# Kernel optimization log

Hardware: AMD Instinct MI355X
Metric: run time of the kernel (lower is better)

The kernel has to match this reference:

```python
import jax, jax.numpy as jnp
import numpy as np

T, N, F_IN, H1, H2, F_OUT = 48, 4096, 64, 64, 32, 64

def setup_inputs() -> dict:
    key = jax.random.key(0)
    ks = jax.random.split(key, 14)
    sc = 0.05
    x = jax.random.normal(ks[0], (T, N, F_IN), jnp.float32)
    adj = jax.random.uniform(ks[1], (N, N), jnp.float32) / N  # roughly row-normalized dense adjacency
    fc_w = jax.random.normal(ks[2], (F_IN, H1), jnp.float32) * sc
    fc_b = jnp.zeros((H1,), jnp.float32)
    Wz = jax.random.normal(ks[3], (H1, F_OUT), jnp.float32) * sc
    Wr = jax.random.normal(ks[4], (H1, F_OUT), jnp.float32) * sc
    Wh = jax.random.normal(ks[5], (H1, F_OUT), jnp.float32) * sc
    Lz = jax.random.normal(ks[6], (2 * F_OUT, F_OUT), jnp.float32) * sc
    Lr = jax.random.normal(ks[7], (2 * F_OUT, F_OUT), jnp.float32) * sc
    Lh = jax.random.normal(ks[8], (2 * F_OUT, F_OUT), jnp.float32) * sc
    bz = jnp.zeros((F_OUT,), jnp.float32)
    br = jnp.zeros((F_OUT,), jnp.float32)
    bh = jnp.zeros((F_OUT,), jnp.float32)
    return {"x": x, "adj": adj, "fc_w": fc_w, "fc_b": fc_b,
            "Wz": Wz, "Wr": Wr, "Wh": Wh,
            "Lz": Lz, "Lr": Lr, "Lh": Lh,
            "bz": bz, "br": br, "bh": bh}

def reference(x, adj, fc_w, fc_b, Wz, Wr, Wh, Lz, Lr, Lh, bz, br, bh):
    # relu(fc(x)) followed by relu(unsqueeze) == single relu
    xh = jax.nn.relu(x @ fc_w + fc_b)          # [T, N, H1]
    h0 = jnp.zeros((N, F_OUT), x.dtype)

    def step(h, xi):
        # TGCN cell: dense graph conv A @ (X W) feeding GRU-style gates
        az = adj @ (xi @ Wz)                   # [N, F_OUT]
        ar = adj @ (xi @ Wr)
        ah = adj @ (xi @ Wh)
        z = jax.nn.sigmoid(jnp.concatenate([az, h], axis=-1) @ Lz + bz)
        r = jax.nn.sigmoid(jnp.concatenate([ar, h], axis=-1) @ Lr + br)
        h_tilde = jnp.tanh(jnp.concatenate([ah, h * r], axis=-1) @ Lh + bh)
        h_new = z * h + (1.0 - z) * h_tilde
        return h_new, None

    h, _ = jax.lax.scan(step, h0, xh)
    return h[None]                              # [1, N, F_OUT]
```

## Files before the change

kernel.cpp:

```cpp
#include <hip/hip_runtime.h>

typedef unsigned short u16;
typedef unsigned char u8;
typedef short s16x8 __attribute__((ext_vector_type(8)));
typedef unsigned short u16x4 __attribute__((ext_vector_type(4)));
typedef float f32x4 __attribute__((ext_vector_type(4)));
typedef int i32x4 __attribute__((ext_vector_type(4)));
typedef int i32x8 __attribute__((ext_vector_type(8)));

#define AS1 __attribute__((address_space(1)))
#define AS3 __attribute__((address_space(3)))

__device__ __forceinline__ void g2l16(const void* g, void* l) {
  __builtin_amdgcn_global_load_lds((const AS1 void*)g, (AS3 void*)l, 16, 0, 0);
}

__device__ __forceinline__ float b2f(u16 u) {
  union { unsigned int i; float f; } x; x.i = ((unsigned int)u) << 16; return x.f;
}
__device__ __forceinline__ u16 f2b(float f) {
  unsigned int u = __builtin_bit_cast(unsigned int, f);
  return (u16)((u + 0x7fffu + ((u >> 16) & 1u)) >> 16);
}
__device__ __forceinline__ u8 f2e4m3(float v) {
  int p = __builtin_amdgcn_cvt_pk_fp8_f32(v, 0.f, 0, false);
  return (u8)(p & 0xff);
}
__device__ __forceinline__ float sigm(float x) { return 1.f / (1.f + __expf(-x)); }
__device__ __forceinline__ float tanh_f(float x) { return 2.f / (1.f + __expf(-2.f * x)) - 1.f; }


__global__ __launch_bounds__(256) void kprep(
    const float* __restrict__ a, u8* __restrict__ ab,
    const float* __restrict__ fcw,
    const float* __restrict__ Wz, const float* __restrict__ Wr, const float* __restrict__ Wh,
    const float* __restrict__ Lz, const float* __restrict__ Lr, const float* __restrict__ Lh,
    u16* __restrict__ fcwT, u16* __restrict__ wct, u16* __restrict__ lbt) {
  int b = blockIdx.x, t = threadIdx.x;
  if (b < 4096) {
    size_t idx = (size_t)b * 256 + t;
    const float4* src = (const float4*)a;
    uint4 o;
    unsigned int r[4];
#pragma unroll
    for (int k = 0; k < 4; ++k) {
      float4 v = src[idx * 4 + k];
      unsigned int p = __builtin_amdgcn_cvt_pk_fp8_f32(v.x * 4096.f, v.y * 4096.f, 0, false);
      p = __builtin_amdgcn_cvt_pk_fp8_f32(v.z * 4096.f, v.w * 4096.f, p, true);
      r[k] = p;
    }
    o.x = r[0]; o.y = r[1]; o.z = r[2]; o.w = r[3];
    ((uint4*)ab)[idx] = o;
    return;
  }
  int bb = b - 4096;
  if (bb < 48) {
    int idx = bb * 256 + t;
    int c_cat = idx >> 6, hh = idx & 63;
    int g = c_cat >> 6, c = c_cat & 63;
    const float* W = (g == 0) ? Wz : (g == 1) ? Wr : Wh;
    const float* L = (g == 0) ? Lz : (g == 1) ? Lr : Lh;
    float acc = 0.f;
    for (int m = 0; m < 64; ++m) acc += W[hh * 64 + m] * L[m * 64 + c];
    wct[c_cat * 64 + hh] = f2b(acc);
  } else if (bb == 48) {
    for (int i = 0; i < 16; ++i) {
      int idx = t * 16 + i; int hh = idx >> 6, f = idx & 63;
      fcwT[hh * 64 + f] = f2b(fcw[f * 64 + hh]);
    }
  } else {
    int g = bb - 49;
    const float* L = (g == 0) ? Lz : (g == 1) ? Lr : Lh;
    for (int i = 0; i < 16; ++i) {
      int idx = t * 16 + i; int c = idx >> 6, hh = idx & 63;
      lbt[g * 4096 + c * 64 + hh] = f2b(L[(64 + hh) * 64 + c]);
    }
  }
}

__global__ __launch_bounds__(256) void k1(
    const float* __restrict__ x, const float* __restrict__ fcb,
    const u16* __restrict__ fcwT, u8* __restrict__ xht) {
  __shared__ __align__(16) u16 xs[128 * 72];
  __shared__ __align__(16) u16 fw[64 * 72];
  __shared__ float fb[64];
  int tid = threadIdx.x, w = tid >> 6, l = tid & 63;
  int t = blockIdx.y, n0 = blockIdx.x * 128;
#pragma unroll
  for (int i2 = 0; i2 < 2; ++i2) {
    int g = tid + 256 * i2;
    s16x8 v = *(const s16x8*)&fcwT[g * 8];
    *(s16x8*)&fw[(g >> 3) * 72 + (g & 7) * 8] = v;
  }
  const float4* xg = (const float4*)(x + ((size_t)t * 4096 + n0) * 64);
#pragma unroll
  for (int i = 0; i < 8; ++i) {
    int s = tid * 8 + i;
    float4 v = xg[s];
    u16x4 p; p[0] = f2b(v.x); p[1] = f2b(v.y); p[2] = f2b(v.z); p[3] = f2b(v.w);
    *(u16x4*)&xs[(s >> 4) * 72 + (s & 15) * 4] = p;
  }
  if (tid < 64) fb[tid] = fcb[tid];
  __syncthreads();

  int lm = l & 15, q = l >> 4;
  f32x4 acc[4][2];
#pragma unroll
  for (int i = 0; i < 4; ++i)
#pragma unroll
    for (int j = 0; j < 2; ++j)
#pragma unroll
      for (int r = 0; r < 4; ++r) acc[i][j][r] = 0.f;
#pragma unroll
  for (int s = 0; s < 2; ++s) {
    s16x8 af[4], bf[2];
#pragma unroll
    for (int i = 0; i < 4; ++i) af[i] = *(const s16x8*)&fw[(16 * i + lm) * 72 + 32 * s + q * 8];
#pragma unroll
    for (int j = 0; j < 2; ++j) bf[j] = *(const s16x8*)&xs[(32 * w + 16 * j + lm) * 72 + 32 * s + q * 8];
#pragma unroll
    for (int i = 0; i < 4; ++i)
#pragma unroll
      for (int j = 0; j < 2; ++j)
        acc[i][j] = __builtin_amdgcn_mfma_f32_16x16x32_bf16(af[i], bf[j], acc[i][j], 0, 0, 0);
  }
#pragma unroll
  for (int i = 0; i < 4; ++i)
#pragma unroll
    for (int j = 0; j < 2; ++j)
#pragma unroll
      for (int r = 0; r < 4; ++r) {
        int h = 16 * i + q * 4 + r;
        int node = 32 * w + 16 * j + lm;
        float v = acc[i][j][r] + fb[h];
        xht[(size_t)(t * 64 + h) * 4096 + n0 + node] = f2e4m3(v > 0.f ? v : 0.f);
      }
}

__global__ __launch_bounds__(256) void k2(
    const u8* __restrict__ A, const u8* __restrict__ B, u16* __restrict__ M) {
  __shared__ __align__(16) u8 As[16384];
  __shared__ __align__(16) u8 Bs[16384];
  int tid = threadIdx.x, w = tid >> 6, l = tid & 63;
  int nt = blockIdx.x, mt = blockIdx.y;
  const u8* Ab = A + (size_t)mt * 128 * 4096;
  const u8* Bb = B + (size_t)nt * 128 * 4096;
  int lm = l & 15, q = l >> 4;
  int wm = w >> 1, wn = w & 1;
  f32x4 acc[4][4];
#pragma unroll
  for (int i = 0; i < 4; ++i)
#pragma unroll
    for (int j = 0; j < 4; ++j)
#pragma unroll
      for (int r = 0; r < 4; ++r) acc[i][j][r] = 0.f;
  for (int k0b = 0; k0b < 4096; k0b += 128) {
#pragma unroll
    for (int j = 0; j < 4; ++j) {
      int r0 = 32 * w + 8 * j;
      int row = r0 + (l >> 3);
      int c = ((l & 7) - row) & 7;
      size_t go = (size_t)row * 4096 + k0b + c * 16;
      g2l16(Ab + go, (char*)As + r0 * 128);
      g2l16(Bb + go, (char*)Bs + r0 * 128);
    }
    __syncthreads();
    i32x8 a8[4], b8[4];
#pragma unroll
    for (int i = 0; i < 4; ++i) {
      int ra = 64 * wm + 16 * i + lm;
      int p0 = (2 * q + ra) & 7, p1 = (2 * q + 1 + ra) & 7;
      i32x4 lo = *(const i32x4*)&As[ra * 128 + p0 * 16];
      i32x4 hi = *(const i32x4*)&As[ra * 128 + p1 * 16];
      a8[i] = __builtin_shufflevector(lo, hi, 0, 1, 2, 3, 4, 5, 6, 7);
      int rb = 64 * wn + 16 * i + lm;
      int q0 = (2 * q + rb) & 7, q1 = (2 * q + 1 + rb) & 7;
      i32x4 lo2 = *(const i32x4*)&Bs[rb * 128 + q0 * 16];
      i32x4 hi2 = *(const i32x4*)&Bs[rb * 128 + q1 * 16];
      b8[i] = __builtin_shufflevector(lo2, hi2, 0, 1, 2, 3, 4, 5, 6, 7);
    }
#pragma unroll
    for (int i = 0; i < 4; ++i)
#pragma unroll
      for (int j = 0; j < 4; ++j)
        acc[i][j] = __builtin_amdgcn_mfma_scale_f32_16x16x128_f8f6f4(
            a8[i], b8[j], acc[i][j], 0, 0, 0, 127, 0, 127);
    __syncthreads();
  }
  const float sc = 1.f / 4096.f;
#pragma unroll
  for (int i = 0; i < 4; ++i)
#pragma unroll
    for (int j = 0; j < 4; ++j)
#pragma unroll
      for (int r = 0; r < 4; ++r) {
        int row = mt * 128 + 64 * wm + 16 * i + q * 4 + r;
        int col = nt * 128 + 64 * wn + 16 * j + lm;
        M[(size_t)row * 3072 + col] = f2b(acc[i][j][r] * sc);
      }
}

__global__ __launch_bounds__(256) void k3(
    const u16* __restrict__ M, const u16* __restrict__ wct, const u16* __restrict__ lbt,
    const float* __restrict__ bz, const float* __restrict__ br, const float* __restrict__ bh,
    float* __restrict__ out) {
  __shared__ __align__(16) u16 hhi[16 * 72], hlo[16 * 72];
  __shared__ __align__(16) u16 rhi[16 * 72], rlo[16 * 72];
  int tid = threadIdx.x, w = tid >> 6, l = tid & 63;
  int nb0 = blockIdx.x * 16;
  int lm = l & 15, q = l >> 4;
  int cb = 16 * w + q * 4;
  s16x8 afw[3][2], afl[3][2];
#pragma unroll
  for (int g = 0; g < 3; ++g)
#pragma unroll
    for (int s = 0; s < 2; ++s) {
      afw[g][s] = *(const s16x8*)&wct[(size_t)(g * 64 + 16 * w + lm) * 64 + 32 * s + q * 8];
      afl[g][s] = *(const s16x8*)&lbt[(size_t)(g * 64 + 16 * w + lm) * 64 + 32 * s + q * 8];
    }
  for (int i = tid; i < 16 * 72; i += 256) { hhi[i] = 0; hlo[i] = 0; }
  f32x4 bzv, brv, bhv, hv;
#pragma unroll
  for (int r = 0; r < 4; ++r) {
    bzv[r] = bz[cb + r]; brv[r] = br[cb + r]; bhv[r] = bh[cb + r]; hv[r] = 0.f;
  }
  __syncthreads();

  const u16* Mrow = M + (size_t)(nb0 + lm) * 3072;
  s16x8 Mn[2];
  Mn[0] = *(const s16x8*)&Mrow[q * 8];
  Mn[1] = *(const s16x8*)&Mrow[32 + q * 8];

  for (int t = 0; t < 48; ++t) {
    s16x8 Mc[2] = {Mn[0], Mn[1]};
    if (t < 47) {
      Mn[0] = *(const s16x8*)&Mrow[(t + 1) * 64 + q * 8];
      Mn[1] = *(const s16x8*)&Mrow[(t + 1) * 64 + 32 + q * 8];
    }
    f32x4 uz, ur;
#pragma unroll
    for (int r = 0; r < 4; ++r) { uz[r] = 0.f; ur[r] = 0.f; }
#pragma unroll
    for (int s = 0; s < 2; ++s) {
      s16x8 hh = *(const s16x8*)&hhi[lm * 72 + 32 * s + q * 8];
      s16x8 hl = *(const s16x8*)&hlo[lm * 72 + 32 * s + q * 8];
      uz = __builtin_amdgcn_mfma_f32_16x16x32_bf16(afw[0][s], Mc[s], uz, 0, 0, 0);
      uz = __builtin_amdgcn_mfma_f32_16x16x32_bf16(afl[0][s], hh, uz, 0, 0, 0);
      uz = __builtin_amdgcn_mfma_f32_16x16x32_bf16(afl[0][s], hl, uz, 0, 0, 0);
      ur = __builtin_amdgcn_mfma_f32_16x16x32_bf16(afw[1][s], Mc[s], ur, 0, 0, 0);
      ur = __builtin_amdgcn_mfma_f32_16x16x32_bf16(afl[1][s], hh, ur, 0, 0, 0);
      ur = __builtin_amdgcn_mfma_f32_16x16x32_bf16(afl[1][s], hl, ur, 0, 0, 0);
    }
    f32x4 zv, rv;
#pragma unroll
    for (int r = 0; r < 4; ++r) {
      zv[r] = sigm(uz[r] + bzv[r]);
      rv[r] = sigm(ur[r] + brv[r]);
    }
    {
      u16x4 phi, plo;
#pragma unroll
      for (int r = 0; r < 4; ++r) {
        float p = hv[r] * rv[r];
        u16 hi = f2b(p); phi[r] = hi; plo[r] = f2b(p - b2f(hi));
      }
      *(u16x4*)&rhi[lm * 72 + cb] = phi;
      *(u16x4*)&rlo[lm * 72 + cb] = plo;
    }
    __syncthreads();
    f32x4 uh;
#pragma unroll
    for (int r = 0; r < 4; ++r) uh[r] = 0.f;
#pragma unroll
    for (int s = 0; s < 2; ++s) {
      s16x8 rh = *(const s16x8*)&rhi[lm * 72 + 32 * s + q * 8];
      s16x8 rl = *(const s16x8*)&rlo[lm * 72 + 32 * s + q * 8];
      uh = __builtin_amdgcn_mfma_f32_16x16x32_bf16(afw[2][s], Mc[s], uh, 0, 0, 0);
      uh = __builtin_amdgcn_mfma_f32_16x16x32_bf16(afl[2][s], rh, uh, 0, 0, 0);
      uh = __builtin_amdgcn_mfma_f32_16x16x32_bf16(afl[2][s], rl, uh, 0, 0, 0);
    }
    {
      u16x4 phi, plo;
#pragma unroll
      for (int r = 0; r < 4; ++r) {
        float th = tanh_f(uh[r] + bhv[r]);
        float hn = zv[r] * hv[r] + (1.f - zv[r]) * th;
        hv[r] = hn;
        u16 hi = f2b(hn); phi[r] = hi; plo[r] = f2b(hn - b2f(hi));
      }
      *(u16x4*)&hhi[lm * 72 + cb] = phi;
      *(u16x4*)&hlo[lm * 72 + cb] = plo;
    }
    __syncthreads();
  }
#pragma unroll
  for (int r = 0; r < 4; ++r)
    out[(size_t)(nb0 + lm) * 64 + cb + r] = hv[r];
}

extern "C" void kernel_launch(void* const* d_in, const int* in_sizes, int n_in,
                              void* d_out, int out_size, void* d_ws, size_t ws_size,
                              hipStream_t stream) {
  const float* x   = (const float*)d_in[0];
  const float* adj = (const float*)d_in[1];
  const float* fcw = (const float*)d_in[2];
  const float* fcb = (const float*)d_in[3];
  const float* Wz  = (const float*)d_in[4];
  const float* Wr  = (const float*)d_in[5];
  const float* Wh  = (const float*)d_in[6];
  const float* Lz  = (const float*)d_in[7];
  const float* Lr  = (const float*)d_in[8];
  const float* Lh  = (const float*)d_in[9];
  const float* bz  = (const float*)d_in[10];
  const float* br  = (const float*)d_in[11];
  const float* bh  = (const float*)d_in[12];
  char* ws = (char*)d_ws;
  u8*  xht  = (u8*)(ws);
  u8*  adj8 = (u8*)(ws + (size_t)12582912);
  u16* Mm   = (u16*)(ws + (size_t)29360128);
  u16* fcwT = (u16*)(ws + (size_t)54525952);
  u16* wct  = (u16*)(ws + (size_t)54534144);
  u16* lbt  = (u16*)(ws + (size_t)54558720);
  float* outp = (float*)d_out;

  hipLaunchKernelGGL(kprep, dim3(4148), dim3(256), 0, stream,
                     adj, adj8, fcw, Wz, Wr, Wh, Lz, Lr, Lh, fcwT, wct, lbt);
  hipLaunchKernelGGL(k1, dim3(32, 48), dim3(256), 0, stream, x, fcb, fcwT, xht);
  hipLaunchKernelGGL(k2, dim3(24, 32), dim3(256), 0, stream, adj8, xht, Mm);
  hipLaunchKernelGGL(k3, dim3(256), dim3(256), 0, stream, Mm, wct, lbt, bz, br, bh, outp);
}
```

Measured before the change: 278.7 us.

## Stage k1 and k2 outputs through LDS for coalesced 16-byte global stores

k1 now writes its fp8 activations into a shared tile and then copies them out as 32-byte contiguous row segments, replacing scattered single-byte global stores. k2 stages its bf16 output tile in the reused A/B shared buffer, one half at a time, and writes full 16-byte vectors per thread instead of strided 2-byte stores. The prep kernel and k1's input loads switch to a strided-by-block indexing so adjacent threads touch adjacent addresses. These changes add extra barriers and shared memory traffic in exchange for coalesced global writes.

```diff
diff --git a/kernel.cpp b/kernel.cpp
--- a/kernel.cpp
+++ b/kernel.cpp
@@ -40,17 +40,14 @@
   if (b < 4096) {
     size_t idx = (size_t)b * 256 + t;
     const float4* src = (const float4*)a;
-    uint4 o;
-    unsigned int r[4];
+    unsigned int* dst = (unsigned int*)ab;
 #pragma unroll
     for (int k = 0; k < 4; ++k) {
-      float4 v = src[idx * 4 + k];
+      float4 v = src[idx + (size_t)k * 1048576];
       unsigned int p = __builtin_amdgcn_cvt_pk_fp8_f32(v.x * 4096.f, v.y * 4096.f, 0, false);
       p = __builtin_amdgcn_cvt_pk_fp8_f32(v.z * 4096.f, v.w * 4096.f, p, true);
-      r[k] = p;
-    }
-    o.x = r[0]; o.y = r[1]; o.z = r[2]; o.w = r[3];
-    ((uint4*)ab)[idx] = o;
+      dst[idx + (size_t)k * 1048576] = p;
+    }
     return;
   }
   int bb = b - 4096;
@@ -83,6 +80,7 @@
     const u16* __restrict__ fcwT, u8* __restrict__ xht) {
   __shared__ __align__(16) u16 xs[128 * 72];
   __shared__ __align__(16) u16 fw[64 * 72];
+  __shared__ __align__(16) u8 xh8[64 * 128];
   __shared__ float fb[64];
   int tid = threadIdx.x, w = tid >> 6, l = tid & 63;
   int t = blockIdx.y, n0 = blockIdx.x * 128;
@@ -95,10 +93,10 @@
   const float4* xg = (const float4*)(x + ((size_t)t * 4096 + n0) * 64);
 #pragma unroll
   for (int i = 0; i < 8; ++i) {
-    int s = tid * 8 + i;
-    float4 v = xg[s];
+    int f = tid + i * 256;
+    float4 v = xg[f];
     u16x4 p; p[0] = f2b(v.x); p[1] = f2b(v.y); p[2] = f2b(v.z); p[3] = f2b(v.w);
-    *(u16x4*)&xs[(s >> 4) * 72 + (s & 15) * 4] = p;
+    *(u16x4*)&xs[(f >> 4) * 72 + (f & 15) * 4] = p;
   }
   if (tid < 64) fb[tid] = fcb[tid];
   __syncthreads();
@@ -127,20 +125,30 @@
 #pragma unroll
   for (int i = 0; i < 4; ++i)
 #pragma unroll
-    for (int j = 0; j < 2; ++j)
+    for (int j = 0; j < 2; ++j) {
+      int node = 32 * w + 16 * j + lm;
+      int h0 = 16 * i + q * 4;
 #pragma unroll
       for (int r = 0; r < 4; ++r) {
-        int h = 16 * i + q * 4 + r;
-        int node = 32 * w + 16 * j + lm;
-        float v = acc[i][j][r] + fb[h];
-        xht[(size_t)(t * 64 + h) * 4096 + n0 + node] = f2e4m3(v > 0.f ? v : 0.f);
+        float v = acc[i][j][r] + fb[h0 + r];
+        xh8[(h0 + r) * 128 + node] = f2e4m3(v > 0.f ? v : 0.f);
       }
+    }
+  __syncthreads();
+  {
+    int h = tid >> 2, seg = tid & 3;
+    u8* dst = xht + (size_t)(t * 64 + h) * 4096 + n0 + seg * 32;
+    const u8* src = &xh8[h * 128 + seg * 32];
+    *(i32x4*)dst = *(const i32x4*)src;
+    *(i32x4*)(dst + 16) = *(const i32x4*)(src + 16);
+  }
 }
 
 __global__ __launch_bounds__(256) void k2(
     const u8* __restrict__ A, const u8* __restrict__ B, u16* __restrict__ M) {
-  __shared__ __align__(16) u8 As[16384];
-  __shared__ __align__(16) u8 Bs[16384];
+  __shared__ __align__(16) u8 sh[32768];
+  u8* As = sh;
+  u8* Bs = sh + 16384;
   int tid = threadIdx.x, w = tid >> 6, l = tid & 63;
   int nt = blockIdx.x, mt = blockIdx.y;
   const u8* Ab = A + (size_t)mt * 128 * 4096;
@@ -187,17 +195,29 @@
             a8[i], b8[j], acc[i][j], 0, 0, 0, 127, 0, 127);
     __syncthreads();
   }
+  u16* tb = (u16*)sh;
   const float sc = 1.f / 4096.f;
 #pragma unroll
-  for (int i = 0; i < 4; ++i)
-#pragma unroll
-    for (int j = 0; j < 4; ++j)
-#pragma unroll
-      for (int r = 0; r < 4; ++r) {
-        int row = mt * 128 + 64 * wm + 16 * i + q * 4 + r;
-        int col = nt * 128 + 64 * wn + 16 * j + lm;
-        M[(size_t)row * 3072 + col] = f2b(acc[i][j][r] * sc);
-      }
+  for (int p = 0; p < 2; ++p) {
+    if (p) __syncthreads();
+    if (wm == p) {
+#pragma unroll
+      for (int i = 0; i < 4; ++i)
+#pragma unroll
+        for (int j = 0; j < 4; ++j)
+#pragma unroll
+          for (int r = 0; r < 4; ++r)
+            tb[(16 * i + 4 * q + r) * 136 + 64 * wn + 16 * j + lm] = f2b(acc[i][j][r] * sc);
+    }
+    __syncthreads();
+    int row = tid >> 2, seg = tid & 3;
+    u16* dst = M + (size_t)(mt * 128 + p * 64 + row) * 3072 + nt * 128 + seg * 32;
+    const u16* src = &tb[row * 136 + seg * 32];
+    *(i32x4*)dst = *(const i32x4*)src;
+    *(i32x4*)(dst + 8)  = *(const i32x4*)(src + 8);
+    *(i32x4*)(dst + 16) = *(const i32x4*)(src + 16);
+    *(i32x4*)(dst + 24) = *(const i32x4*)(src + 24);
+  }
 }
 
 __global__ __launch_bounds__(256) void k3(
```

Result: no change. 282.9 us (+1.5%).
